# Performance work log

Measured on AMD Instinct MI355X. Metric: run time of the kernel, lower is better.

The kernel has to match this reference:

```python
import jax, jax.numpy as jnp
import numpy as np

IN_DIM = 128
HID = 128
NUM_CLASSES = 10
N_NODES = 100000
N_EDGES = 1600000
NUM_GRAPHS = 128


def setup_inputs() -> dict:
    key = jax.random.key(0)
    ks = jax.random.split(key, 12)
    X = jax.random.normal(ks[0], (N_NODES, IN_DIM), dtype=jnp.float32)
    EI = jax.random.randint(ks[1], (2, N_EDGES), 0, N_NODES, dtype=jnp.int64)
    batch = jnp.sort(jax.random.randint(ks[2], (N_NODES,), 0, NUM_GRAPHS, dtype=jnp.int64))
    s_in = 1.0 / np.sqrt(IN_DIM)
    s_h = 1.0 / np.sqrt(HID)
    s_m = 1.0 / np.sqrt(2 * HID)
    params = {
        'W1': jax.random.uniform(ks[3], (IN_DIM, HID), jnp.float32, -s_in, s_in),
        'b1': jnp.zeros((HID,), jnp.float32),
        'W2': jax.random.uniform(ks[4], (HID, HID), jnp.float32, -s_h, s_h),
        'b2': jnp.zeros((HID,), jnp.float32),
        'W3': jax.random.uniform(ks[5], (HID, HID), jnp.float32, -s_h, s_h),
        'b3': jnp.zeros((HID,), jnp.float32),
        'Wm1': jax.random.uniform(ks[6], (2 * HID, HID), jnp.float32, -s_m, s_m),
        'bm1': jnp.zeros((HID,), jnp.float32),
        'Wm2': jax.random.uniform(ks[7], (HID, NUM_CLASSES), jnp.float32, -s_h, s_h),
        'bm2': jnp.zeros((NUM_CLASSES,), jnp.float32),
    }
    return dict(X=X, EI=EI, batch=batch, num_graphs=NUM_GRAPHS, **params)


def _gcn_norm(EI, n):
    # add self loops, compute D^{-1/2}[row] * D^{-1/2}[col]
    loops = jnp.arange(n, dtype=EI.dtype)
    row = jnp.concatenate([EI[0], loops])
    col = jnp.concatenate([EI[1], loops])
    deg = jax.ops.segment_sum(jnp.ones_like(row, dtype=jnp.float32), row, num_segments=n)
    dis = (deg + 1e-12) ** -0.5
    norm = dis[row] * dis[col]
    return row, col, norm


def _gcn_layer(x, row, col, norm, W, b):
    h = x @ W + b                       # [N, out]
    msg = h[col] * norm[:, None]        # gather + scale  [E+N, out]
    return jax.ops.segment_sum(msg, row, num_segments=x.shape[0])  # scatter-add


def _pool_mean_max(x, batch, num_graphs):
    s = jax.ops.segment_sum(x, batch, num_segments=num_graphs)
    cnt = jax.ops.segment_sum(jnp.ones((x.shape[0],), x.dtype), batch, num_segments=num_graphs)
    mean = s / (cnt[:, None] + 1e-12)
    mx = jax.ops.segment_max(x, batch, num_segments=num_graphs)
    return jnp.concatenate([mean, mx], axis=1)


def reference(X, EI, batch, num_graphs, W1, b1, W2, b2, W3, b3, Wm1, bm1, Wm2, bm2):
    n = X.shape[0]
    row, col, norm = _gcn_norm(EI, n)
    x = jax.nn.relu(_gcn_layer(X, row, col, norm, W1, b1))
    x = jax.nn.relu(_gcn_layer(x, row, col, norm, W2, b2))
    x = jax.nn.relu(_gcn_layer(x, row, col, norm, W3, b3))
    g = _pool_mean_max(x, batch, num_graphs)
    h = jax.nn.relu(g @ Wm1 + bm1)
    return h @ Wm2 + bm2
```

## Files before the change

### kernel.cpp

```cpp
#include <hip/hip_runtime.h>
#include <hip/hip_fp16.h>
#include <cstdint>
#include <cstddef>

#define DIM 128
#define NG 128
#define NCLS 10
#define PSLICE 8
#define CPAD 64
#define NOWN 256
#define RPB 391
#define NPBLK 1024
#define OCAP 16
#define OVCAP 65536

typedef _Float16 f16;
typedef __attribute__((ext_vector_type(8))) _Float16 f16x8;
typedef __attribute__((ext_vector_type(4))) float f32x4;


__global__ __launch_bounds__(256) void k_part(
    const int* __restrict__ rw, const int* __restrict__ cl, int E,
    unsigned* __restrict__ buckets, int* __restrict__ bcnt,
    unsigned long long* __restrict__ ovf, int* __restrict__ ovfn) {
  __shared__ int lcnt[NOWN];
  if (threadIdx.x < NOWN) lcnt[threadIdx.x] = 0;
  __syncthreads();
  int b = blockIdx.x;
  int C = (((E + NPBLK - 1) / NPBLK + 3) & ~3);
  int s = b * C;
  int e = s + C;
  if (e > E) e = E;
  auto put = [&](int r, int c) {
    int o = (unsigned)r / RPB;
    int li = r - o * RPB;
    int sl = atomicAdd(&lcnt[o], 1);
    if (sl < OCAP) {
      buckets[((size_t)o * NPBLK + b) * OCAP + sl] =
          ((unsigned)li << 17) | (unsigned)c;
    } else {
      int oi = atomicAdd(ovfn, 1);
      if (oi < OVCAP)
        ovf[oi] = ((unsigned long long)(unsigned)r << 32) | (unsigned)c;
    }
  };
  for (int i = s + (int)threadIdx.x * 4; i < e; i += 1024) {
    if (i + 3 < e) {
      int4 r4 = *(const int4*)(rw + i);
      int4 c4 = *(const int4*)(cl + i);
      put(r4.x, c4.x);
      put(r4.y, c4.y);
      put(r4.z, c4.z);
      put(r4.w, c4.w);
    } else {
      for (int j = i; j < e; ++j) put(rw[j], cl[j]);
    }
  }
  __syncthreads();
  if (threadIdx.x < NOWN) {
    int v = lcnt[threadIdx.x];
    bcnt[threadIdx.x * NPBLK + b] = v < OCAP ? v : OCAP;
  }
}

__global__ __launch_bounds__(256) void k_place(
    const unsigned* __restrict__ buckets, const int* __restrict__ bcnt,
    const unsigned long long* __restrict__ ovf, const int* __restrict__ ovfn,
    int* __restrict__ cnt, float* __restrict__ dis, int* __restrict__ csrc,
    int N) {
  extern __shared__ int sm[];
  int* lcnt = sm;
  int* csr = sm + ((RPB + 3) & ~3);
  int o = blockIdx.x;
  int r0 = o * RPB;
  int rows = N - r0;
  if (rows > RPB) rows = RPB;
  if (rows <= 0) return;
  for (int i = threadIdx.x; i < rows; i += 256) lcnt[i] = 0;
  __syncthreads();
  const int* bc = bcnt + o * NPBLK;
  const unsigned* bp = buckets + (size_t)o * NPBLK * OCAP;
  for (int j = (int)threadIdx.x; j < NPBLK * OCAP; j += 256) {
    int seg = j >> 4;
    int pos = j & 15;
    if (pos < bc[seg]) {
      unsigned ent = bp[j];
      int li = (int)(ent >> 17);
      int c = (int)(ent & 0x1ffffu);
      int sl = atomicAdd(&lcnt[li], 1);
      if (sl < CPAD) csr[(li << 6) + sl] = c;
    }
  }
  int nov = *ovfn;
  if (nov > OVCAP) nov = OVCAP;
  for (int j = (int)threadIdx.x; j < nov; j += 256) {
    unsigned long long ent = ovf[j];
    int r = (int)(unsigned)(ent >> 32);
    int li = r - r0;
    if (li >= 0 && li < rows) {
      int c = (int)(unsigned)(ent & 0xffffffffu);
      int sl = atomicAdd(&lcnt[li], 1);
      if (sl < CPAD) csr[(li << 6) + sl] = c;
    }
  }
  __syncthreads();
  uint4* dst = (uint4*)(csrc + ((size_t)r0 << 6));
  const uint4* src = (const uint4*)csr;
  int n4 = rows * 16;
  for (int j = (int)threadIdx.x; j < n4; j += 256) dst[j] = src[j];
  for (int i = threadIdx.x; i < rows; i += 256) {
    int v = lcnt[i];
    cnt[r0 + i] = v;
    dis[r0 + i] = rsqrtf((float)(v + 1));
  }
}

__global__ void k_wt(const float* __restrict__ W1, const float* __restrict__ W2,
                     const float* __restrict__ W3, __half* __restrict__ Wt1,
                     __half* __restrict__ Wt2, __half* __restrict__ Wt3) {
  int gi = blockIdx.x * 256 + threadIdx.x;
  int m = gi / (DIM * DIM);
  int i = gi % (DIM * DIM);
  const float* W = (m == 0) ? W1 : (m == 1) ? W2 : W3;
  __half* Wt = (m == 0) ? Wt1 : (m == 1) ? Wt2 : Wt3;
  int k = i >> 7, c = i & 127;
  Wt[(size_t)c * DIM + k] = __float2half(W[(size_t)k * DIM + c]);
}


template <int FP32IN>
__global__ __launch_bounds__(256, 3) void k_gemm(
    const void* __restrict__ Ain, const __half* __restrict__ Wt,
    const float* __restrict__ bias, const float* __restrict__ dis,
    __half* __restrict__ Hh, int N) {
  int t = threadIdx.x;
  int lane = t & 63;
  int wv = t >> 6;
  int l15 = lane & 15, lg = lane >> 4;
  int cb = (wv & 1) * 64;

  f16x8 bfr[4][4];
#pragma unroll
  for (int ct = 0; ct < 4; ++ct) {
    int c = cb + ct * 16 + l15;
    const f16* wp = (const f16*)Wt + (size_t)c * DIM + lg * 8;
#pragma unroll
    for (int ks = 0; ks < 4; ++ks) bfr[ks][ct] = *(const f16x8*)(wp + ks * 32);
  }
  float bv[4];
#pragma unroll
  for (int ct = 0; ct < 4; ++ct) bv[ct] = bias[cb + ct * 16 + l15];

  const int nt2 = (N + 31) / 32;
  for (int t2 = blockIdx.x; t2 < nt2; t2 += gridDim.x) {
    int row0 = t2 * 32 + (wv >> 1) * 16;
    int rA = row0 + l15;
    if (rA > N - 1) rA = N - 1;
    f16x8 afr[4];
    if constexpr (FP32IN) {
      const float* ap = (const float*)Ain + (size_t)rA * DIM + lg * 8;
#pragma unroll
      for (int ks = 0; ks < 4; ++ks) {
        float4 v0 = *(const float4*)(ap + ks * 32);
        float4 v1 = *(const float4*)(ap + ks * 32 + 4);
        f16x8 a;
        a[0] = (f16)v0.x; a[1] = (f16)v0.y; a[2] = (f16)v0.z; a[3] = (f16)v0.w;
        a[4] = (f16)v1.x; a[5] = (f16)v1.y; a[6] = (f16)v1.z; a[7] = (f16)v1.w;
        afr[ks] = a;
      }
    } else {
      const f16* ap = (const f16*)Ain + (size_t)rA * DIM + lg * 8;
#pragma unroll
      for (int ks = 0; ks < 4; ++ks) afr[ks] = *(const f16x8*)(ap + ks * 32);
    }

    f32x4 acc[4];
#pragma unroll
    for (int ct = 0; ct < 4; ++ct) acc[ct] = (f32x4){0.f, 0.f, 0.f, 0.f};
#pragma unroll
    for (int ks = 0; ks < 4; ++ks)
#pragma unroll
      for (int ct = 0; ct < 4; ++ct)
        acc[ct] = __builtin_amdgcn_mfma_f32_16x16x32_f16(afr[ks], bfr[ks][ct], acc[ct], 0, 0, 0);

#pragma unroll
    for (int j = 0; j < 4; ++j) {
      int r = row0 + lg * 4 + j;
      if (r < N) {
        float dr = dis[r];
#pragma unroll
        for (int ct = 0; ct < 4; ++ct) {
          float o = (acc[ct][j] + bv[ct]) * dr;
          Hh[(size_t)r * DIM + cb + ct * 16 + l15] = __float2half(o);
        }
      }
    }
  }
}


__global__ __launch_bounds__(256) void k_agg(
    const __half* __restrict__ Hh, __half* __restrict__ Ah,
    const int* __restrict__ csrc, const int* __restrict__ cntA,
    const float* __restrict__ dis, int N) {
  int wave = (int)(((size_t)blockIdx.x * blockDim.x + threadIdx.x) >> 6);
  int lane = threadIdx.x & 63;
  int g = lane >> 4;
  int q = lane & 15;
  int r = wave * 4 + g;
  if (r >= N) return;
  int cnt = cntA[r];
  if (cnt > CPAD) cnt = CPAD;
  float dr = dis[r];
  const int* cp = csrc + ((size_t)r << 6);
  const f16* hb = (const f16*)Hh + q * 8;

  float4 aA0 = {0,0,0,0}, aA1 = {0,0,0,0};
  float4 aB0 = {0,0,0,0}, aB1 = {0,0,0,0};
  float4 aC0 = {0,0,0,0}, aC1 = {0,0,0,0};
  float4 aD0 = {0,0,0,0}, aD1 = {0,0,0,0};

#define ACC8(u, x0, x1)                                                   \
  {                                                                       \
    float2 f_;                                                            \
    f_ = __half22float2(*reinterpret_cast<const __half2*>(&(u).x));       \
    x0.x += f_.x; x0.y += f_.y;                                           \
    f_ = __half22float2(*reinterpret_cast<const __half2*>(&(u).y));       \
    x0.z += f_.x; x0.w += f_.y;                                           \
    f_ = __half22float2(*reinterpret_cast<const __half2*>(&(u).z));       \
    x1.x += f_.x; x1.y += f_.y;                                           \
    f_ = __half22float2(*reinterpret_cast<const __half2*>(&(u).w));       \
    x1.z += f_.x; x1.w += f_.y;                                           \
  }

  int i = 0;
  for (; i + 3 < cnt; i += 4) {
    int c0 = cp[i], c1 = cp[i + 1], c2 = cp[i + 2], c3 = cp[i + 3];
    uint4 u0 = *(const uint4*)(hb + (size_t)c0 * DIM);
    uint4 u1 = *(const uint4*)(hb + (size_t)c1 * DIM);
    uint4 u2 = *(const uint4*)(hb + (size_t)c2 * DIM);
    uint4 u3 = *(const uint4*)(hb + (size_t)c3 * DIM);
    ACC8(u0, aA0, aA1);
    ACC8(u1, aB0, aB1);
    ACC8(u2, aC0, aC1);
    ACC8(u3, aD0, aD1);
  }
  for (; i < cnt; ++i) {
    int c0 = cp[i];
    uint4 u0 = *(const uint4*)(hb + (size_t)c0 * DIM);
    ACC8(u0, aA0, aA1);
  }
  {
    uint4 us = *(const uint4*)(hb + (size_t)r * DIM);
    ACC8(us, aA0, aA1);
  }
#undef ACC8
  float4 s0, s1;
  s0.x = (aA0.x + aB0.x) + (aC0.x + aD0.x);
  s0.y = (aA0.y + aB0.y) + (aC0.y + aD0.y);
  s0.z = (aA0.z + aB0.z) + (aC0.z + aD0.z);
  s0.w = (aA0.w + aB0.w) + (aC0.w + aD0.w);
  s1.x = (aA1.x + aB1.x) + (aC1.x + aD1.x);
  s1.y = (aA1.y + aB1.y) + (aC1.y + aD1.y);
  s1.z = (aA1.z + aB1.z) + (aC1.z + aD1.z);
  s1.w = (aA1.w + aB1.w) + (aC1.w + aD1.w);
  float o0 = fmaxf(dr * s0.x, 0.f), o1 = fmaxf(dr * s0.y, 0.f);
  float o2 = fmaxf(dr * s0.z, 0.f), o3 = fmaxf(dr * s0.w, 0.f);
  float o4 = fmaxf(dr * s1.x, 0.f), o5 = fmaxf(dr * s1.y, 0.f);
  float o6 = fmaxf(dr * s1.z, 0.f), o7 = fmaxf(dr * s1.w, 0.f);
  __half2 p0 = __floats2half2_rn(o0, o1);
  __half2 p1 = __floats2half2_rn(o2, o3);
  __half2 p2 = __floats2half2_rn(o4, o5);
  __half2 p3 = __floats2half2_rn(o6, o7);
  uint4 u;
  u.x = *(unsigned int*)&p0;
  u.y = *(unsigned int*)&p1;
  u.z = *(unsigned int*)&p2;
  u.w = *(unsigned int*)&p3;
  *(uint4*)((f16*)Ah + (size_t)r * DIM + q * 8) = u;
}


__device__ __forceinline__ int lower_bound_batch(const int* batch, int N, int g) {
  int lo = 0, hi = N;
  while (lo < hi) {
    int mid = (lo + hi) >> 1;
    if (batch[mid] < g) lo = mid + 1; else hi = mid;
  }
  return lo;
}

__global__ void k_pool1(const __half* __restrict__ A, const int* __restrict__ batch,
                        int N, float* __restrict__ part) {
  int g = blockIdx.x / PSLICE, sl = blockIdx.x % PSLICE;
  int c = threadIdx.x;
  int s = lower_bound_batch(batch, N, g);
  int e = lower_bound_batch(batch, N, g + 1);
  int len = e - s;
  int ns = s + (len * sl) / PSLICE;
  int ne = s + (len * (sl + 1)) / PSLICE;
  float sum = 0.f, mx = -INFINITY;
  for (int n = ns; n < ne; ++n) {
    float v = __half2float(A[(size_t)n * DIM + c]);
    sum += v;
    mx = fmaxf(mx, v);
  }
  part[((size_t)(g * PSLICE + sl) * 2 + 0) * DIM + c] = sum;
  part[((size_t)(g * PSLICE + sl) * 2 + 1) * DIM + c] = mx;
}

__global__ void k_head(const float* __restrict__ part, const int* __restrict__ batch,
                       int N, const float* __restrict__ Wm1,
                       const float* __restrict__ bm1, const float* __restrict__ Wm2,
                       const float* __restrict__ bm2, float* __restrict__ out) {
  __shared__ float gs[256];
  __shared__ float hs[DIM];
  int g = blockIdx.x;
  int c = threadIdx.x;
  float sum = 0.f, mx = -INFINITY;
  for (int sl = 0; sl < PSLICE; ++sl) {
    sum += part[((size_t)(g * PSLICE + sl) * 2 + 0) * DIM + c];
    mx = fmaxf(mx, part[((size_t)(g * PSLICE + sl) * 2 + 1) * DIM + c]);
  }
  int s = lower_bound_batch(batch, N, g);
  int e = lower_bound_batch(batch, N, g + 1);
  gs[c] = sum / ((float)(e - s) + 1e-12f);
  gs[c + 128] = mx;
  __syncthreads();
  float acc = bm1[c];
#pragma unroll 8
  for (int k = 0; k < 256; ++k) acc = fmaf(gs[k], Wm1[k * DIM + c], acc);
  hs[c] = fmaxf(acc, 0.f);
  __syncthreads();
  if (c < NCLS) {
    float a2 = bm2[c];
#pragma unroll 8
    for (int k = 0; k < DIM; ++k) a2 = fmaf(hs[k], Wm2[k * NCLS + c], a2);
    out[(size_t)g * NCLS + c] = a2;
  }
}


static inline size_t al256(size_t x) { return (x + 255) & ~(size_t)255; }

extern "C" void kernel_launch(void* const* d_in, const int* in_sizes, int n_in,
                              void* d_out, int out_size, void* d_ws, size_t ws_size,
                              hipStream_t stream) {
  const float* X = (const float*)d_in[0];
  const int* EI = (const int*)d_in[1];
  const int* batch = (const int*)d_in[2];
  const float* W1 = (const float*)d_in[4];
  const float* b1 = (const float*)d_in[5];
  const float* W2 = (const float*)d_in[6];
  const float* b2 = (const float*)d_in[7];
  const float* W3 = (const float*)d_in[8];
  const float* b3 = (const float*)d_in[9];
  const float* Wm1 = (const float*)d_in[10];
  const float* bm1 = (const float*)d_in[11];
  const float* Wm2 = (const float*)d_in[12];
  const float* bm2 = (const float*)d_in[13];
  float* OUT = (float*)d_out;

  const int N = in_sizes[0] / DIM;
  const int E = in_sizes[1] / 2;
  const int G = NG;

  const int* EI_row = EI;
  const int* EI_col = EI + E;

  char* p = (char*)d_ws;
  size_t off = 0;
  auto take = [&](size_t bytes) { void* r = p + off; off = al256(off + bytes); return r; };

  int* cnt = (int*)take((size_t)N * 4);
  int* bcnt = (int*)take((size_t)NOWN * NPBLK * 4);
  int* ovfn = (int*)take(256);
  unsigned long long* ovf = (unsigned long long*)take((size_t)OVCAP * 8);
  float* dis = (float*)take((size_t)N * 4);
  int* csrc = (int*)take((size_t)N * CPAD * 4);
  unsigned* buckets = (unsigned*)take((size_t)NOWN * NPBLK * OCAP * 4);
  __half* Hh = (__half*)take((size_t)N * DIM * 2);
  __half* Ah = (__half*)take((size_t)N * DIM * 2);
  __half* Wt1 = (__half*)take((size_t)DIM * DIM * 2);
  __half* Wt2 = (__half*)take((size_t)DIM * DIM * 2);
  __half* Wt3 = (__half*)take((size_t)DIM * DIM * 2);
  float* part = (float*)take((size_t)G * PSLICE * 2 * DIM * 4);
  (void)ws_size; (void)n_in; (void)out_size;

  hipMemsetAsync(ovfn, 0, 4, stream);

  k_part<<<NPBLK, 256, 0, stream>>>(EI_row, EI_col, E, buckets, bcnt, ovf, ovfn);
  const int placeLds = ((RPB + 3) & ~3) * 4 + RPB * 64 * 4;
  k_place<<<NOWN, 256, placeLds, stream>>>(buckets, bcnt, ovf, ovfn, cnt, dis, csrc, N);
  k_wt<<<192, 256, 0, stream>>>(W1, W2, W3, Wt1, Wt2, Wt3);

  const int aggBlocks = (N * 16 + 255) / 256;

  k_gemm<1><<<1024, 256, 0, stream>>>(X, Wt1, b1, dis, Hh, N);
  k_agg<<<aggBlocks, 256, 0, stream>>>(Hh, Ah, csrc, cnt, dis, N);
  k_gemm<0><<<1024, 256, 0, stream>>>(Ah, Wt2, b2, dis, Hh, N);
  k_agg<<<aggBlocks, 256, 0, stream>>>(Hh, Ah, csrc, cnt, dis, N);
  k_gemm<0><<<1024, 256, 0, stream>>>(Ah, Wt3, b3, dis, Hh, N);
  k_agg<<<aggBlocks, 256, 0, stream>>>(Hh, Ah, csrc, cnt, dis, N);

  k_pool1<<<G * PSLICE, DIM, 0, stream>>>(Ah, batch, N, part);
  k_head<<<G, DIM, 0, stream>>>(part, batch, N, Wm1, bm1, Wm2, bm2, OUT);
}
```

Baseline: 369.3 us.

## Fold weight transpose into partition kernel, add nontemporal stores, halve GEMM grid

Merges the weight-transpose kernel into the edge-partition launch as extra blocks, which removes one kernel launch. The CSR copy-out and the final aggregation output now use nontemporal stores to reduce cache pollution. The GEMM grid drops from 1024 to 512 blocks, so each block presumably loops over more row tiles. Nontemporal stores on the last aggregation could slow the pool kernel if it would have hit in cache, and the smaller GEMM grid may reduce occupancy.

```diff
diff --git a/kernel.cpp b/kernel.cpp
--- a/kernel.cpp
+++ b/kernel.cpp
@@ -11,18 +11,33 @@
 #define NOWN 256
 #define RPB 391
 #define NPBLK 1024
+#define WTBLK 192
 #define OCAP 16
 #define OVCAP 65536
 
 typedef _Float16 f16;
 typedef __attribute__((ext_vector_type(8))) _Float16 f16x8;
 typedef __attribute__((ext_vector_type(4))) float f32x4;
+typedef __attribute__((ext_vector_type(4))) unsigned u32x4;
 
 
 __global__ __launch_bounds__(256) void k_part(
     const int* __restrict__ rw, const int* __restrict__ cl, int E,
     unsigned* __restrict__ buckets, int* __restrict__ bcnt,
-    unsigned long long* __restrict__ ovf, int* __restrict__ ovfn) {
+    unsigned long long* __restrict__ ovf, int* __restrict__ ovfn,
+    const float* __restrict__ W1, const float* __restrict__ W2,
+    const float* __restrict__ W3, __half* __restrict__ Wt1,
+    __half* __restrict__ Wt2, __half* __restrict__ Wt3) {
+  if (blockIdx.x >= NPBLK) {
+    int gi = (blockIdx.x - NPBLK) * 256 + threadIdx.x;
+    int m = gi / (DIM * DIM);
+    int i = gi % (DIM * DIM);
+    const float* W = (m == 0) ? W1 : (m == 1) ? W2 : W3;
+    __half* Wt = (m == 0) ? Wt1 : (m == 1) ? Wt2 : Wt3;
+    int k = i >> 7, c = i & 127;
+    Wt[(size_t)c * DIM + k] = __float2half(W[(size_t)k * DIM + c]);
+    return;
+  }
   __shared__ int lcnt[NOWN];
   if (threadIdx.x < NOWN) lcnt[threadIdx.x] = 0;
   __syncthreads();
@@ -104,27 +119,16 @@
     }
   }
   __syncthreads();
-  uint4* dst = (uint4*)(csrc + ((size_t)r0 << 6));
-  const uint4* src = (const uint4*)csr;
+  u32x4* dst = (u32x4*)(csrc + ((size_t)r0 << 6));
+  const u32x4* src = (const u32x4*)csr;
   int n4 = rows * 16;
-  for (int j = (int)threadIdx.x; j < n4; j += 256) dst[j] = src[j];
+  for (int j = (int)threadIdx.x; j < n4; j += 256)
+    __builtin_nontemporal_store(src[j], dst + j);
   for (int i = threadIdx.x; i < rows; i += 256) {
     int v = lcnt[i];
     cnt[r0 + i] = v;
     dis[r0 + i] = rsqrtf((float)(v + 1));
   }
-}
-
-__global__ void k_wt(const float* __restrict__ W1, const float* __restrict__ W2,
-                     const float* __restrict__ W3, __half* __restrict__ Wt1,
-                     __half* __restrict__ Wt2, __half* __restrict__ Wt3) {
-  int gi = blockIdx.x * 256 + threadIdx.x;
-  int m = gi / (DIM * DIM);
-  int i = gi % (DIM * DIM);
-  const float* W = (m == 0) ? W1 : (m == 1) ? W2 : W3;
-  __half* Wt = (m == 0) ? Wt1 : (m == 1) ? Wt2 : Wt3;
-  int k = i >> 7, c = i & 127;
-  Wt[(size_t)c * DIM + k] = __float2half(W[(size_t)k * DIM + c]);
 }
 
 
@@ -199,6 +203,7 @@
 }
 
 
+template <int STORE_NT>
 __global__ __launch_bounds__(256) void k_agg(
     const __half* __restrict__ Hh, __half* __restrict__ Ah,
     const int* __restrict__ csrc, const int* __restrict__ cntA,
@@ -272,12 +277,17 @@
   __half2 p1 = __floats2half2_rn(o2, o3);
   __half2 p2 = __floats2half2_rn(o4, o5);
   __half2 p3 = __floats2half2_rn(o6, o7);
-  uint4 u;
+  u32x4 u;
   u.x = *(unsigned int*)&p0;
   u.y = *(unsigned int*)&p1;
   u.z = *(unsigned int*)&p2;
   u.w = *(unsigned int*)&p3;
-  *(uint4*)((f16*)Ah + (size_t)r * DIM + q * 8) = u;
+  u32x4* dst = (u32x4*)((f16*)Ah + (size_t)r * DIM + q * 8);
+  if constexpr (STORE_NT) {
+    __builtin_nontemporal_store(u, dst);
+  } else {
+    *dst = u;
+  }
 }
 
 
@@ -389,19 +399,19 @@
 
   hipMemsetAsync(ovfn, 0, 4, stream);
 
-  k_part<<<NPBLK, 256, 0, stream>>>(EI_row, EI_col, E, buckets, bcnt, ovf, ovfn);
+  k_part<<<NPBLK + WTBLK, 256, 0, stream>>>(EI_row, EI_col, E, buckets, bcnt,
+                                            ovf, ovfn, W1, W2, W3, Wt1, Wt2, Wt3);
   const int placeLds = ((RPB + 3) & ~3) * 4 + RPB * 64 * 4;
   k_place<<<NOWN, 256, placeLds, stream>>>(buckets, bcnt, ovf, ovfn, cnt, dis, csrc, N);
-  k_wt<<<192, 256, 0, stream>>>(W1, W2, W3, Wt1, Wt2, Wt3);
 
   const int aggBlocks = (N * 16 + 255) / 256;
 
-  k_gemm<1><<<1024, 256, 0, stream>>>(X, Wt1, b1, dis, Hh, N);
-  k_agg<<<aggBlocks, 256, 0, stream>>>(Hh, Ah, csrc, cnt, dis, N);
-  k_gemm<0><<<1024, 256, 0, stream>>>(Ah, Wt2, b2, dis, Hh, N);
-  k_agg<<<aggBlocks, 256, 0, stream>>>(Hh, Ah, csrc, cnt, dis, N);
-  k_gemm<0><<<1024, 256, 0, stream>>>(Ah, Wt3, b3, dis, Hh, N);
-  k_agg<<<aggBlocks, 256, 0, stream>>>(Hh, Ah, csrc, cnt, dis, N);
+  k_gemm<1><<<512, 256, 0, stream>>>(X, Wt1, b1, dis, Hh, N);
+  k_agg<0><<<aggBlocks, 256, 0, stream>>>(Hh, Ah, csrc, cnt, dis, N);
+  k_gemm<0><<<512, 256, 0, stream>>>(Ah, Wt2, b2, dis, Hh, N);
+  k_agg<0><<<aggBlocks, 256, 0, stream>>>(Hh, Ah, csrc, cnt, dis, N);
+  k_gemm<0><<<512, 256, 0, stream>>>(Ah, Wt3, b3, dis, Hh, N);
+  k_agg<1><<<aggBlocks, 256, 0, stream>>>(Hh, Ah, csrc, cnt, dis, N);
 
   k_pool1<<<G * PSLICE, DIM, 0, stream>>>(Ah, batch, N, part);
   k_head<<<G, DIM, 0, stream>>>(part, batch, N, Wm1, bm1, Wm2, bm2, OUT);
```

After: 378.3 us. 1.02x slower.
